# Performance work log

Hardware: AMD Instinct MI355X
Metric: run time of the kernel (lower is better)

## Reference

```python
import jax, jax.numpy as jnp
import numpy as np

EPS = 1e-5

def _sort(pts, idx):
    # torch.gather(pts, 1, idx[..., None].expand(-1, -1, C))
    return jnp.take_along_axis(pts, idx[:, :, None], axis=1)

def _ln(x, gamma, beta):
    m = x.mean(-1, keepdims=True)
    v = x.var(-1, keepdims=True)  # ddof=0, matches torch LayerNorm
    return (x - m) / jnp.sqrt(v + EPS) * gamma + beta


def setup_inputs() -> dict:
    key = jax.random.key(0)
    ks = jax.random.split(key, 8)
    B, N, dim, rank = 16, 8192, 384, 64
    g, s = 128, 64  # group_num, group_size; N = g*s
    inp = jax.random.normal(ks[0], (B, N, dim), dtype=jnp.float32)
    sub_U = jax.random.normal(ks[1], (2, B, g, s, s), dtype=jnp.float32) / np.sqrt(s)
    idx = jax.random.randint(ks[2], (2, B, N), 0, N, dtype=jnp.int64)
    Wd = jax.random.normal(ks[3], (rank, dim), dtype=jnp.float32) * np.sqrt(2.0 / (dim + rank))
    bd = jnp.zeros((rank,), jnp.float32)
    # note: original zero-inits up/adapt1; use small random so grads are non-degenerate
    Wu = jax.random.normal(ks[4], (dim, rank), dtype=jnp.float32) * 0.02
    bu = jnp.zeros((dim,), jnp.float32)
    Wa = jax.random.normal(ks[5], (rank, rank), dtype=jnp.float32) * 0.02
    ba = jnp.zeros((rank,), jnp.float32)
    gamma = jnp.ones((rank,), jnp.float32)
    beta = jnp.zeros((rank,), jnp.float32)
    return {"input": inp, "sub_U": sub_U, "idx": idx, "Wd": Wd, "bd": bd,
            "Wu": Wu, "bu": bu, "Wa": Wa, "ba": ba, "gamma": gamma, "beta": beta}


def reference(input, sub_U, idx, Wd, bd, Wu, bu, Wa, ba, gamma, beta):
    B, N, _ = input.shape
    _, _, g, s, _ = sub_U.shape
    r = Wd.shape[0]
    h = jax.nn.silu(input @ Wd.T + bd)                       # down + act, [B,N,r]

    sub_x = _sort(h, idx[0]).reshape(B, g, s, r)             # gather + group

    def branch(U, sx):
        # U^T @ x  -> [B,g,s,r]
        f = jnp.einsum('bgts,bgtr->bgsr', U, sx)
        # residual zero-init adapter: f + silu(adapt1(LN(f)))
        f = f + jax.nn.silu(_ln(f, gamma, beta) @ Wa.T + ba)
        # U @ f -> back to point space, flatten groups
        return jnp.einsum('bgst,bgtr->bgsr', U, f).reshape(B, g * s, r)

    # branch 0's result is overwritten in the original code (dead), kept for fidelity
    y0 = branch(sub_U[0], sub_x)
    _dead = _sort(y0, idx[1])

    y1 = branch(sub_U[1], sub_x)
    x = _sort(y1, idx[1]) + y1
    h = x + h
    return h @ Wu.T + bu
```

## Files before the change

### kernel.cpp

```cpp
#include <hip/hip_runtime.h>

#define NN    8192
#define DD    384
#define RR    64
#define BNROW 131072
#define NGRP  2048

typedef __attribute__((ext_vector_type(8))) short short8;
typedef __attribute__((ext_vector_type(4))) float floatx4;

__device__ __forceinline__ float silu_f(float x) {
    return x / (1.0f + __expf(-x));
}

__device__ __forceinline__ unsigned bf2(float a, float b) {
    unsigned ua = __float_as_uint(a), ub = __float_as_uint(b);
    ua = (ua + 0x7fffu + ((ua >> 16) & 1u)) >> 16;
    ub = (ub + 0x7fffu + ((ub >> 16) & 1u)) >> 16;
    return ua | (ub << 16);
}

union S8 { unsigned u[4]; short8 s; };

__global__ __launch_bounds__(256) void kA(const float* __restrict__ in,
                                          const float* __restrict__ Wd,
                                          const float* __restrict__ bd,
                                          float* __restrict__ h) {
    __shared__ unsigned short WdB[64 * 392];
    const int tid = threadIdx.x;
    for (int i = tid; i < 6144; i += 256) {
        int n = i / 96, c4 = i - n * 96;
        float4 v = *(const float4*)(Wd + n * DD + c4 * 4);
        *(uint2*)&WdB[n * 392 + c4 * 4] = make_uint2(bf2(v.x, v.y), bf2(v.z, v.w));
    }
    __syncthreads();

    const int lane = tid & 63, w = tid >> 6;
    const int quad = lane >> 4, lr = lane & 15;
    const int grow = blockIdx.x * 64 + w * 16 + lr;
    const float* arow = in + grow * DD;

    floatx4 acc[4] = {};
    #pragma unroll
    for (int ks = 0; ks < 12; ++ks) {
        float4 p = *(const float4*)(arow + ks * 32 + quad * 8);
        float4 q = *(const float4*)(arow + ks * 32 + quad * 8 + 4);
        S8 a;
        a.u[0] = bf2(p.x, p.y); a.u[1] = bf2(p.z, p.w);
        a.u[2] = bf2(q.x, q.y); a.u[3] = bf2(q.z, q.w);
        #pragma unroll
        for (int n = 0; n < 4; ++n) {
            const short8 b = *(const short8*)&WdB[(n * 16 + lr) * 392 + ks * 32 + quad * 8];
            acc[n] = __builtin_amdgcn_mfma_f32_16x16x32_bf16(a.s, b, acc[n], 0, 0, 0);
        }
    }
    const int orow0 = blockIdx.x * 64 + w * 16 + quad * 4;
    #pragma unroll
    for (int n = 0; n < 4; ++n) {
        float bb = bd[n * 16 + lr];
        #pragma unroll
        for (int i = 0; i < 4; ++i)
            h[(orow0 + i) * 64 + n * 16 + lr] = silu_f(acc[n][i] + bb);
    }
}

#define MAC16(AS, BS, ACC, K) \
  { float a0_=AS[(K)*65+4*ty+0], a1_=AS[(K)*65+4*ty+1], a2_=AS[(K)*65+4*ty+2], a3_=AS[(K)*65+4*ty+3]; \
    float b0_=BS[(K)*65+4*tx+0], b1_=BS[(K)*65+4*tx+1], b2_=BS[(K)*65+4*tx+2], b3_=BS[(K)*65+4*tx+3]; \
    ACC[0][0]+=a0_*b0_; ACC[0][1]+=a0_*b1_; ACC[0][2]+=a0_*b2_; ACC[0][3]+=a0_*b3_; \
    ACC[1][0]+=a1_*b0_; ACC[1][1]+=a1_*b1_; ACC[1][2]+=a1_*b2_; ACC[1][3]+=a1_*b3_; \
    ACC[2][0]+=a2_*b0_; ACC[2][1]+=a2_*b1_; ACC[2][2]+=a2_*b2_; ACC[2][3]+=a2_*b3_; \
    ACC[3][0]+=a3_*b0_; ACC[3][1]+=a3_*b1_; ACC[3][2]+=a3_*b2_; ACC[3][3]+=a3_*b3_; }

__global__ __launch_bounds__(256) void kB(const float* __restrict__ h,
                                          const float* __restrict__ U1,
                                          const int*   __restrict__ idx0,
                                          const float* __restrict__ Wa,
                                          const float* __restrict__ ba,
                                          const float* __restrict__ gamma,
                                          const float* __restrict__ beta,
                                          float* __restrict__ y1) {
    __shared__ float UA[64*65];
    __shared__ float XF[64*65];
    __shared__ float WT[64*65];
    const int tid = threadIdx.x;
    const int tx = tid & 15, ty = tid >> 4;
    const int bg = blockIdx.x;
    const int b  = bg >> 7;
    const float* U = U1 + bg * 4096;

    for (int it = 0; it < 4; ++it) {
        int idx = it * 256 + tid;
        int row = idx >> 4;
        int kq  = idx & 15;
        float4 u = *(const float4*)(U + row * 64 + kq * 4);
        UA[row*65 + kq*4+0] = u.x;
        UA[row*65 + kq*4+1] = u.y;
        UA[row*65 + kq*4+2] = u.z;
        UA[row*65 + kq*4+3] = u.w;
        int src = idx0[bg * 64 + row];
        float4 x = *(const float4*)(h + (b * NN + src) * 64 + kq * 4);
        XF[row*65 + kq*4+0] = x.x;
        XF[row*65 + kq*4+1] = x.y;
        XF[row*65 + kq*4+2] = x.z;
        XF[row*65 + kq*4+3] = x.w;
        float4 w = *(const float4*)(Wa + row * 64 + kq * 4);
        WT[(kq*4+0)*65 + row] = w.x;
        WT[(kq*4+1)*65 + row] = w.y;
        WT[(kq*4+2)*65 + row] = w.z;
        WT[(kq*4+3)*65 + row] = w.w;
    }
    __syncthreads();

    float f[4][4] = {};
    #pragma unroll 8
    for (int t = 0; t < 64; ++t) {
        MAC16(UA, XF, f, t);
    }
    __syncthreads();

    const float g0 = gamma[4*tx+0], g1 = gamma[4*tx+1], g2 = gamma[4*tx+2], g3 = gamma[4*tx+3];
    const float e0 = beta[4*tx+0],  e1 = beta[4*tx+1],  e2 = beta[4*tx+2],  e3 = beta[4*tx+3];
    float lnv[4][4];
    #pragma unroll
    for (int i = 0; i < 4; ++i) {
        float sm = f[i][0] + f[i][1] + f[i][2] + f[i][3];
        float sq = f[i][0]*f[i][0] + f[i][1]*f[i][1] + f[i][2]*f[i][2] + f[i][3]*f[i][3];
        #pragma unroll
        for (int mask = 1; mask <= 8; mask <<= 1) {
            sm += __shfl_xor(sm, mask, 64);
            sq += __shfl_xor(sq, mask, 64);
        }
        float mean = sm * 0.015625f;
        float var  = sq * 0.015625f - mean * mean;
        float rstd = rsqrtf(var + 1e-5f);
        lnv[i][0] = (f[i][0] - mean) * rstd * g0 + e0;
        lnv[i][1] = (f[i][1] - mean) * rstd * g1 + e1;
        lnv[i][2] = (f[i][2] - mean) * rstd * g2 + e2;
        lnv[i][3] = (f[i][3] - mean) * rstd * g3 + e3;
    }
    #pragma unroll
    for (int i = 0; i < 4; ++i)
        #pragma unroll
        for (int j = 0; j < 4; ++j)
            UA[(4*tx+j)*65 + (4*ty+i)] = lnv[i][j];
    __syncthreads();

    float a[4][4] = {};
    #pragma unroll 8
    for (int r = 0; r < 64; ++r) {
        MAC16(UA, WT, a, r);
    }
    const float a0 = ba[4*tx+0], a1 = ba[4*tx+1], a2 = ba[4*tx+2], a3 = ba[4*tx+3];
    #pragma unroll
    for (int i = 0; i < 4; ++i) {
        f[i][0] += silu_f(a[i][0] + a0);
        f[i][1] += silu_f(a[i][1] + a1);
        f[i][2] += silu_f(a[i][2] + a2);
        f[i][3] += silu_f(a[i][3] + a3);
    }
    __syncthreads();

    for (int it = 0; it < 4; ++it) {
        int idx = it * 256 + tid;
        int row = idx >> 4;
        int kq  = idx & 15;
        float4 u = *(const float4*)(U + row * 64 + kq * 4);
        UA[(kq*4+0)*65 + row] = u.x;
        UA[(kq*4+1)*65 + row] = u.y;
        UA[(kq*4+2)*65 + row] = u.z;
        UA[(kq*4+3)*65 + row] = u.w;
    }
    #pragma unroll
    for (int i = 0; i < 4; ++i)
        #pragma unroll
        for (int j = 0; j < 4; ++j)
            XF[(4*ty+i)*65 + 4*tx+j] = f[i][j];
    __syncthreads();

    float y[4][4] = {};
    #pragma unroll 8
    for (int t = 0; t < 64; ++t) {
        MAC16(UA, XF, y, t);
    }
    for (int i = 0; i < 4; ++i) {
        float4 o;
        o.x = y[i][0]; o.y = y[i][1]; o.z = y[i][2]; o.w = y[i][3];
        *(float4*)(y1 + (bg * 64 + 4*ty + i) * 64 + 4*tx) = o;
    }
}

__global__ __launch_bounds__(256) void kC(const float* __restrict__ h,
                                          const float* __restrict__ y1,
                                          const int*   __restrict__ idx1,
                                          const float* __restrict__ Wu,
                                          const float* __restrict__ bu,
                                          float* __restrict__ out) {
    __shared__ unsigned short WuB[384 * 72];
    __shared__ unsigned short Xs[64 * 72];
    const int tid = threadIdx.x;
    const int m0 = blockIdx.x * 64;
    const int b  = m0 >> 13;
    const int n0 = m0 & (NN - 1);

    for (int i = tid; i < 6144; i += 256) {
        int n = i >> 4, c4 = i & 15;
        float4 v = *(const float4*)(Wu + n * 64 + c4 * 4);
        *(uint2*)&WuB[n * 72 + c4 * 4] = make_uint2(bf2(v.x, v.y), bf2(v.z, v.w));
    }
    #pragma unroll
    for (int it = 0; it < 4; ++it) {
        int idx = it * 256 + tid;
        int r = idx >> 4, kq = idx & 15;
        int i1 = idx1[b * NN + n0 + r];
        const float4 ya = *(const float4*)(y1 + (b * NN + i1) * 64 + kq * 4);
        const float4 yb = *(const float4*)(y1 + (m0 + r) * 64 + kq * 4);
        const float4 hh = *(const float4*)(h  + (m0 + r) * 64 + kq * 4);
        *(uint2*)&Xs[r * 72 + kq * 4] =
            make_uint2(bf2(ya.x + yb.x + hh.x, ya.y + yb.y + hh.y),
                       bf2(ya.z + yb.z + hh.z, ya.w + yb.w + hh.w));
    }
    __syncthreads();

    const int lane = tid & 63, w = tid >> 6;
    const int quad = lane >> 4, lr = lane & 15;
    const short8 a0 = *(const short8*)&Xs[(w * 16 + lr) * 72 + quad * 8];
    const short8 a1 = *(const short8*)&Xs[(w * 16 + lr) * 72 + 32 + quad * 8];
    const int orow0 = m0 + w * 16 + quad * 4;

    #pragma unroll
    for (int nt = 0; nt < 24; ++nt) {
        const short8 b0 = *(const short8*)&WuB[(nt * 16 + lr) * 72 + quad * 8];
        const short8 b1 = *(const short8*)&WuB[(nt * 16 + lr) * 72 + 32 + quad * 8];
        floatx4 d = {};
        d = __builtin_amdgcn_mfma_f32_16x16x32_bf16(a0, b0, d, 0, 0, 0);
        d = __builtin_amdgcn_mfma_f32_16x16x32_bf16(a1, b1, d, 0, 0, 0);
        const float bb = bu[nt * 16 + lr];
        #pragma unroll
        for (int i = 0; i < 4; ++i)
            out[(orow0 + i) * DD + nt * 16 + lr] = d[i] + bb;
    }
}

extern "C" void kernel_launch(void* const* d_in, const int* in_sizes, int n_in,
                              void* d_out, int out_size, void* d_ws, size_t ws_size,
                              hipStream_t stream) {
    const float* input = (const float*)d_in[0];
    const float* subU  = (const float*)d_in[1];
    const int*   idx   = (const int*)  d_in[2];
    const float* Wd    = (const float*)d_in[3];
    const float* bd    = (const float*)d_in[4];
    const float* Wu    = (const float*)d_in[5];
    const float* bu    = (const float*)d_in[6];
    const float* Wa    = (const float*)d_in[7];
    const float* ba    = (const float*)d_in[8];
    const float* gamma = (const float*)d_in[9];
    const float* beta  = (const float*)d_in[10];
    float* out = (float*)d_out;

    float* h  = (float*)d_ws;
    float* y1 = h + 8388608;

    const float* U1   = subU + 8388608;
    const int*   idx0 = idx;
    const int*   idx1 = idx + BNROW;

    kA<<<2048, 256, 0, stream>>>(input, Wd, bd, h);
    kB<<<2048, 256, 0, stream>>>(h, U1, idx0, Wa, ba, gamma, beta, y1);
    kC<<<2048, 256, 0, stream>>>(h, y1, idx1, Wu, bu, out);
}
```

Before: 515.7 us.

## Move group matmuls to split-bf16 MFMA and precompute bf16 weights

```diff
diff --git a/kernel.cpp b/kernel.cpp
--- a/kernel.cpp
+++ b/kernel.cpp
@@ -13,44 +13,59 @@
     return x / (1.0f + __expf(-x));
 }
 
+__device__ __forceinline__ unsigned bfr(float x) {
+    unsigned u = __float_as_uint(x);
+    return (u + 0x7fffu + ((u >> 16) & 1u)) >> 16;
+}
+
 __device__ __forceinline__ unsigned bf2(float a, float b) {
-    unsigned ua = __float_as_uint(a), ub = __float_as_uint(b);
-    ua = (ua + 0x7fffu + ((ua >> 16) & 1u)) >> 16;
-    ub = (ub + 0x7fffu + ((ub >> 16) & 1u)) >> 16;
-    return ua | (ub << 16);
+    return bfr(a) | (bfr(b) << 16);
 }
 
 union S8 { unsigned u[4]; short8 s; };
 
+__global__ __launch_bounds__(256) void kP(const float* __restrict__ Wd,
+                                          const float* __restrict__ Wu,
+                                          const float* __restrict__ Wa,
+                                          unsigned short* __restrict__ WdB,
+                                          unsigned short* __restrict__ WuB,
+                                          unsigned short* __restrict__ WaB) {
+    int i = blockIdx.x * 256 + threadIdx.x;
+    const float* s;
+    unsigned short* d;
+    if (i < 6144)        { s = Wd + i * 4;           d = WdB + i * 4; }
+    else if (i < 12288)  { s = Wu + (i - 6144) * 4;  d = WuB + (i - 6144) * 4; }
+    else                 { s = Wa + (i - 12288) * 4; d = WaB + (i - 12288) * 4; }
+    float4 v = *(const float4*)s;
+    *(uint2*)d = make_uint2(bf2(v.x, v.y), bf2(v.z, v.w));
+}
+
 __global__ __launch_bounds__(256) void kA(const float* __restrict__ in,
-                                          const float* __restrict__ Wd,
+                                          const unsigned short* __restrict__ WdB,
                                           const float* __restrict__ bd,
                                           float* __restrict__ h) {
-    __shared__ unsigned short WdB[64 * 392];
     const int tid = threadIdx.x;
-    for (int i = tid; i < 6144; i += 256) {
-        int n = i / 96, c4 = i - n * 96;
-        float4 v = *(const float4*)(Wd + n * DD + c4 * 4);
-        *(uint2*)&WdB[n * 392 + c4 * 4] = make_uint2(bf2(v.x, v.y), bf2(v.z, v.w));
-    }
-    __syncthreads();
-
     const int lane = tid & 63, w = tid >> 6;
     const int quad = lane >> 4, lr = lane & 15;
     const int grow = blockIdx.x * 64 + w * 16 + lr;
-    const float* arow = in + grow * DD;
+    const float* arow = in + grow * DD + quad * 8;
+
+    float4 v0[12], v1[12];
+    #pragma unroll
+    for (int ks = 0; ks < 12; ++ks) {
+        v0[ks] = *(const float4*)(arow + ks * 32);
+        v1[ks] = *(const float4*)(arow + ks * 32 + 4);
+    }
 
     floatx4 acc[4] = {};
     #pragma unroll
     for (int ks = 0; ks < 12; ++ks) {
-        float4 p = *(const float4*)(arow + ks * 32 + quad * 8);
-        float4 q = *(const float4*)(arow + ks * 32 + quad * 8 + 4);
         S8 a;
-        a.u[0] = bf2(p.x, p.y); a.u[1] = bf2(p.z, p.w);
-        a.u[2] = bf2(q.x, q.y); a.u[3] = bf2(q.z, q.w);
-        #pragma unroll
-        for (int n = 0; n < 4; ++n) {
-            const short8 b = *(const short8*)&WdB[(n * 16 + lr) * 392 + ks * 32 + quad * 8];
+        a.u[0] = bf2(v0[ks].x, v0[ks].y); a.u[1] = bf2(v0[ks].z, v0[ks].w);
+        a.u[2] = bf2(v1[ks].x, v1[ks].y); a.u[3] = bf2(v1[ks].z, v1[ks].w);
+        #pragma unroll
+        for (int n = 0; n < 4; ++n) {
+            const short8 b = *(const short8*)&WdB[(n * 16 + lr) * DD + ks * 32 + quad * 8];
             acc[n] = __builtin_amdgcn_mfma_f32_16x16x32_bf16(a.s, b, acc[n], 0, 0, 0);
         }
     }
@@ -63,69 +78,72 @@
             h[(orow0 + i) * 64 + n * 16 + lr] = silu_f(acc[n][i] + bb);
     }
 }
-
-#define MAC16(AS, BS, ACC, K) \
-  { float a0_=AS[(K)*65+4*ty+0], a1_=AS[(K)*65+4*ty+1], a2_=AS[(K)*65+4*ty+2], a3_=AS[(K)*65+4*ty+3]; \
-    float b0_=BS[(K)*65+4*tx+0], b1_=BS[(K)*65+4*tx+1], b2_=BS[(K)*65+4*tx+2], b3_=BS[(K)*65+4*tx+3]; \
-    ACC[0][0]+=a0_*b0_; ACC[0][1]+=a0_*b1_; ACC[0][2]+=a0_*b2_; ACC[0][3]+=a0_*b3_; \
-    ACC[1][0]+=a1_*b0_; ACC[1][1]+=a1_*b1_; ACC[1][2]+=a1_*b2_; ACC[1][3]+=a1_*b3_; \
-    ACC[2][0]+=a2_*b0_; ACC[2][1]+=a2_*b1_; ACC[2][2]+=a2_*b2_; ACC[2][3]+=a2_*b3_; \
-    ACC[3][0]+=a3_*b0_; ACC[3][1]+=a3_*b1_; ACC[3][2]+=a3_*b2_; ACC[3][3]+=a3_*b3_; }
 
 __global__ __launch_bounds__(256) void kB(const float* __restrict__ h,
                                           const float* __restrict__ U1,
                                           const int*   __restrict__ idx0,
-                                          const float* __restrict__ Wa,
+                                          const unsigned short* __restrict__ WaB,
                                           const float* __restrict__ ba,
                                           const float* __restrict__ gamma,
                                           const float* __restrict__ beta,
                                           float* __restrict__ y1) {
-    __shared__ float UA[64*65];
-    __shared__ float XF[64*65];
-    __shared__ float WT[64*65];
+    __shared__ unsigned short AH[64 * 72];
+    __shared__ unsigned short AL[64 * 72];
+    __shared__ unsigned short BH[64 * 72];
+    __shared__ unsigned short BL[64 * 72];
     const int tid = threadIdx.x;
-    const int tx = tid & 15, ty = tid >> 4;
-    const int bg = blockIdx.x;
+    const int bg = ((blockIdx.x & 7) << 8) | (blockIdx.x >> 3);
     const int b  = bg >> 7;
     const float* U = U1 + bg * 4096;
 
+    #pragma unroll
     for (int it = 0; it < 4; ++it) {
         int idx = it * 256 + tid;
         int row = idx >> 4;
         int kq  = idx & 15;
         float4 u = *(const float4*)(U + row * 64 + kq * 4);
-        UA[row*65 + kq*4+0] = u.x;
-        UA[row*65 + kq*4+1] = u.y;
-        UA[row*65 + kq*4+2] = u.z;
-        UA[row*65 + kq*4+3] = u.w;
         int src = idx0[bg * 64 + row];
         float4 x = *(const float4*)(h + (b * NN + src) * 64 + kq * 4);
-        XF[row*65 + kq*4+0] = x.x;
-        XF[row*65 + kq*4+1] = x.y;
-        XF[row*65 + kq*4+2] = x.z;
-        XF[row*65 + kq*4+3] = x.w;
-        float4 w = *(const float4*)(Wa + row * 64 + kq * 4);
-        WT[(kq*4+0)*65 + row] = w.x;
-        WT[(kq*4+1)*65 + row] = w.y;
-        WT[(kq*4+2)*65 + row] = w.z;
-        WT[(kq*4+3)*65 + row] = w.w;
+        float uv[4] = {u.x, u.y, u.z, u.w};
+        float xv[4] = {x.x, x.y, x.z, x.w};
+        #pragma unroll
+        for (int j = 0; j < 4; ++j) {
+            unsigned uh = bfr(uv[j]);
+            AH[(4 * kq + j) * 72 + row] = (unsigned short)uh;
+            AL[(4 * kq + j) * 72 + row] = (unsigned short)bfr(uv[j] - __uint_as_float(uh << 16));
+            unsigned xh = bfr(xv[j]);
+            BH[(4 * kq + j) * 72 + row] = (unsigned short)xh;
+            BL[(4 * kq + j) * 72 + row] = (unsigned short)bfr(xv[j] - __uint_as_float(xh << 16));
+        }
     }
     __syncthreads();
 
-    float f[4][4] = {};
-    #pragma unroll 8
-    for (int t = 0; t < 64; ++t) {
-        MAC16(UA, XF, f, t);
-    }
-    __syncthreads();
-
-    const float g0 = gamma[4*tx+0], g1 = gamma[4*tx+1], g2 = gamma[4*tx+2], g3 = gamma[4*tx+3];
-    const float e0 = beta[4*tx+0],  e1 = beta[4*tx+1],  e2 = beta[4*tx+2],  e3 = beta[4*tx+3];
-    float lnv[4][4];
+    const int lane = tid & 63, w = tid >> 6;
+    const int quad = lane >> 4, lr = lane & 15;
+    const int mrow = w * 16 + lr;
+
+    floatx4 f[4] = {};
+    #pragma unroll
+    for (int k = 0; k < 2; ++k) {
+        const short8 aH = *(const short8*)&AH[mrow * 72 + k * 32 + quad * 8];
+        const short8 aL = *(const short8*)&AL[mrow * 72 + k * 32 + quad * 8];
+        #pragma unroll
+        for (int n = 0; n < 4; ++n) {
+            const short8 bh = *(const short8*)&BH[(n * 16 + lr) * 72 + k * 32 + quad * 8];
+            const short8 bl = *(const short8*)&BL[(n * 16 + lr) * 72 + k * 32 + quad * 8];
+            f[n] = __builtin_amdgcn_mfma_f32_16x16x32_bf16(aH, bh, f[n], 0, 0, 0);
+            f[n] = __builtin_amdgcn_mfma_f32_16x16x32_bf16(aH, bl, f[n], 0, 0, 0);
+            f[n] = __builtin_amdgcn_mfma_f32_16x16x32_bf16(aL, bh, f[n], 0, 0, 0);
+        }
+    }
+
+    float gv[4], bv[4];
+    #pragma unroll
+    for (int n = 0; n < 4; ++n) { gv[n] = gamma[n * 16 + lr]; bv[n] = beta[n * 16 + lr]; }
     #pragma unroll
     for (int i = 0; i < 4; ++i) {
-        float sm = f[i][0] + f[i][1] + f[i][2] + f[i][3];
-        float sq = f[i][0]*f[i][0] + f[i][1]*f[i][1] + f[i][2]*f[i][2] + f[i][3]*f[i][3];
+        float sm = f[0][i] + f[1][i] + f[2][i] + f[3][i];
+        float sq = f[0][i]*f[0][i] + f[1][i]*f[1][i] + f[2][i]*f[2][i] + f[3][i]*f[3][i];
         #pragma unroll
         for (int mask = 1; mask <= 8; mask <<= 1) {
             sm += __shfl_xor(sm, mask, 64);
@@ -134,80 +152,97 @@
         float mean = sm * 0.015625f;
         float var  = sq * 0.015625f - mean * mean;
         float rstd = rsqrtf(var + 1e-5f);
-        lnv[i][0] = (f[i][0] - mean) * rstd * g0 + e0;
-        lnv[i][1] = (f[i][1] - mean) * rstd * g1 + e1;
-        lnv[i][2] = (f[i][2] - mean) * rstd * g2 + e2;
-        lnv[i][3] = (f[i][3] - mean) * rstd * g3 + e3;
-    }
-    #pragma unroll
-    for (int i = 0; i < 4; ++i)
-        #pragma unroll
-        for (int j = 0; j < 4; ++j)
-            UA[(4*tx+j)*65 + (4*ty+i)] = lnv[i][j];
+        int srow = w * 16 + quad * 4 + i;
+        #pragma unroll
+        for (int n = 0; n < 4; ++n) {
+            float ln = (f[n][i] - mean) * rstd * gv[n] + bv[n];
+            AH[srow * 72 + n * 16 + lr] = (unsigned short)bfr(ln);
+        }
+    }
+
+    floatx4 av[4] = {};
+    #pragma unroll
+    for (int k = 0; k < 2; ++k) {
+        const short8 a2 = *(const short8*)&AH[mrow * 72 + k * 32 + quad * 8];
+        #pragma unroll
+        for (int n = 0; n < 4; ++n) {
+            const short8 bw = *(const short8*)&WaB[(n * 16 + lr) * 64 + k * 32 + quad * 8];
+            av[n] = __builtin_amdgcn_mfma_f32_16x16x32_bf16(a2, bw, av[n], 0, 0, 0);
+        }
+    }
+    float bav[4];
+    #pragma unroll
+    for (int n = 0; n < 4; ++n) bav[n] = ba[n * 16 + lr];
+    #pragma unroll
+    for (int n = 0; n < 4; ++n)
+        #pragma unroll
+        for (int i = 0; i < 4; ++i)
+            f[n][i] += silu_f(av[n][i] + bav[n]);
+
     __syncthreads();
 
-    float a[4][4] = {};
-    #pragma unroll 8
-    for (int r = 0; r < 64; ++r) {
-        MAC16(UA, WT, a, r);
-    }
-    const float a0 = ba[4*tx+0], a1 = ba[4*tx+1], a2 = ba[4*tx+2], a3 = ba[4*tx+3];
-    #pragma unroll
-    for (int i = 0; i < 4; ++i) {
-        f[i][0] += silu_f(a[i][0] + a0);
-        f[i][1] += silu_f(a[i][1] + a1);
-        f[i][2] += silu_f(a[i][2] + a2);
-        f[i][3] += silu_f(a[i][3] + a3);
+    #pragma unroll
+    for (int n = 0; n < 4; ++n)
+        #pragma unroll
+        for (int i = 0; i < 4; ++i) {
+            float v = f[n][i];
+            unsigned hb = bfr(v);
+            BH[(n * 16 + lr) * 72 + w * 16 + quad * 4 + i] = (unsigned short)hb;
+            BL[(n * 16 + lr) * 72 + w * 16 + quad * 4 + i] =
+                (unsigned short)bfr(v - __uint_as_float(hb << 16));
+        }
+    #pragma unroll
+    for (int c = 0; c < 4; ++c) {
+        float4 u = *(const float4*)(U + mrow * 64 + quad * 16 + c * 4);
+        float uv[4] = {u.x, u.y, u.z, u.w};
+        unsigned hh[4], ll[4];
+        #pragma unroll
+        for (int j = 0; j < 4; ++j) {
+            hh[j] = bfr(uv[j]);
+            ll[j] = bfr(uv[j] - __uint_as_float(hh[j] << 16));
+        }
+        *(uint2*)&AH[mrow * 72 + quad * 16 + c * 4] =
+            make_uint2(hh[0] | (hh[1] << 16), hh[2] | (hh[3] << 16));
+        *(uint2*)&AL[mrow * 72 + quad * 16 + c * 4] =
+            make_uint2(ll[0] | (ll[1] << 16), ll[2] | (ll[3] << 16));
     }
     __syncthreads();
 
-    for (int it = 0; it < 4; ++it) {
-        int idx = it * 256 + tid;
-        int row = idx >> 4;
-        int kq  = idx & 15;
-        float4 u = *(const float4*)(U + row * 64 + kq * 4);
-        UA[(kq*4+0)*65 + row] = u.x;
-        UA[(kq*4+1)*65 + row] = u.y;
-        UA[(kq*4+2)*65 + row] = u.z;
-        UA[(kq*4+3)*65 + row] = u.w;
-    }
-    #pragma unroll
-    for (int i = 0; i < 4; ++i)
-        #pragma unroll
-        for (int j = 0; j < 4; ++j)
-            XF[(4*ty+i)*65 + 4*tx+j] = f[i][j];
-    __syncthreads();
-
-    float y[4][4] = {};
-    #pragma unroll 8
-    for (int t = 0; t < 64; ++t) {
-        MAC16(UA, XF, y, t);
-    }
-    for (int i = 0; i < 4; ++i) {
-        float4 o;
-        o.x = y[i][0]; o.y = y[i][1]; o.z = y[i][2]; o.w = y[i][3];
-        *(float4*)(y1 + (bg * 64 + 4*ty + i) * 64 + 4*tx) = o;
-    }
+    floatx4 y[4] = {};
+    #pragma unroll
+    for (int k = 0; k < 2; ++k) {
+        const short8 aH = *(const short8*)&AH[mrow * 72 + k * 32 + quad * 8];
+        const short8 aL = *(const short8*)&AL[mrow * 72 + k * 32 + quad * 8];
+        #pragma unroll
+        for (int n = 0; n < 4; ++n) {
+            const short8 bh = *(const short8*)&BH[(n * 16 + lr) * 72 + k * 32 + quad * 8];
+            const short8 bl = *(const short8*)&BL[(n * 16 + lr) * 72 + k * 32 + quad * 8];
+            y[n] = __builtin_amdgcn_mfma_f32_16x16x32_bf16(aH, bh, y[n], 0, 0, 0);
+            y[n] = __builtin_amdgcn_mfma_f32_16x16x32_bf16(aH, bl, y[n], 0, 0, 0);
+            y[n] = __builtin_amdgcn_mfma_f32_16x16x32_bf16(aL, bh, y[n], 0, 0, 0);
+        }
+    }
+    const int orow = bg * 64 + w * 16 + quad * 4;
+    #pragma unroll
+    for (int n = 0; n < 4; ++n)
+        #pragma unroll
+        for (int i = 0; i < 4; ++i)
+            y1[(orow + i) * 64 + n * 16 + lr] = y[n][i];
 }
 
 __global__ __launch_bounds__(256) void kC(const float* __restrict__ h,
                                           const float* __restrict__ y1,
                                           const int*   __restrict__ idx1,
-                                          const float* __restrict__ Wu,
+                                          const unsigned short* __restrict__ WuB,
                                           const float* __restrict__ bu,
                                           float* __restrict__ out) {
-    __shared__ unsigned short WuB[384 * 72];
     __shared__ unsigned short Xs[64 * 72];
     const int tid = threadIdx.x;
-    const int m0 = blockIdx.x * 64;
+    const int bid = ((blockIdx.x & 7) << 8) | (blockIdx.x >> 3);
+    const int m0 = bid * 64;
     const int b  = m0 >> 13;
     const int n0 = m0 & (NN - 1);
 
-    for (int i = tid; i < 6144; i += 256) {
-        int n = i >> 4, c4 = i & 15;
-        float4 v = *(const float4*)(Wu + n * 64 + c4 * 4);
-        *(uint2*)&WuB[n * 72 + c4 * 4] = make_uint2(bf2(v.x, v.y), bf2(v.z, v.w));
-    }
     #pragma unroll
     for (int it = 0; it < 4; ++it) {
         int idx = it * 256 + tid;
@@ -230,8 +265,8 @@
 
     #pragma unroll
     for (int nt = 0; nt < 24; ++nt) {
-        const short8 b0 = *(const short8*)&WuB[(nt * 16 + lr) * 72 + quad * 8];
-        const short8 b1 = *(const short8*)&WuB[(nt * 16 + lr) * 72 + 32 + quad * 8];
+        const short8 b0 = *(const short8*)&WuB[(nt * 16 + lr) * 64 + quad * 8];
+        const short8 b1 = *(const short8*)&WuB[(nt * 16 + lr) * 64 + 32 + quad * 8];
         floatx4 d = {};
         d = __builtin_amdgcn_mfma_f32_16x16x32_bf16(a0, b0, d, 0, 0, 0);
         d = __builtin_amdgcn_mfma_f32_16x16x32_bf16(a1, b1, d, 0, 0, 0);
@@ -260,12 +295,16 @@
 
     float* h  = (float*)d_ws;
     float* y1 = h + 8388608;
+    unsigned short* WdB = (unsigned short*)(y1 + 8388608);
+    unsigned short* WuB = WdB + 24576;
+    unsigned short* WaB = WuB + 24576;
 
     const float* U1   = subU + 8388608;
     const int*   idx0 = idx;
     const int*   idx1 = idx + BNROW;
 
-    kA<<<2048, 256, 0, stream>>>(input, Wd, bd, h);
-    kB<<<2048, 256, 0, stream>>>(h, U1, idx0, Wa, ba, gamma, beta, y1);
-    kC<<<2048, 256, 0, stream>>>(h, y1, idx1, Wu, bu, out);
-}
+    kP<<<52,   256, 0, stream>>>(Wd, Wu, Wa, WdB, WuB, WaB);
+    kA<<<2048, 256, 0, stream>>>(input, WdB, bd, h);
+    kB<<<2048, 256, 0, stream>>>(h, U1, idx0, WaB, ba, gamma, beta, y1);
+    kC<<<2048, 256, 0, stream>>>(h, y1, idx1, WuB, bu, out);
+}
```

Result: faster. 492.1 us (-4.6%).
